# Kernel optimization log

Measured on AMD Instinct MI355X. Metric: run time of the kernel, lower is better.

## Reference

```python
import jax, jax.numpy as jnp
import numpy as np

B, N, D, S, H = 128, 4096, 64, 7, 128  # batch, tokens, slot_size, num_slots, mlp_hidden
EPS = 1e-8
LN_EPS = 1e-5


def _ln(x, w, b):
    m = jnp.mean(x, axis=-1, keepdims=True)
    v = jnp.mean((x - m) ** 2, axis=-1, keepdims=True)
    return (x - m) * jax.lax.rsqrt(v + LN_EPS) * w + b


def setup_inputs() -> dict:
    key = jax.random.key(0)
    ks = jax.random.split(key, 12)
    glorot = lambda k, shape: jax.random.normal(k, shape, jnp.float32) * (2.0 / sum(shape)) ** 0.5
    return {
        "inputs": jax.random.normal(ks[0], (B, N, D), jnp.float32),
        "slots_noise": jax.random.normal(ks[1], (B, S, D), jnp.float32),
        "ln_in_w": jnp.ones((D,), jnp.float32), "ln_in_b": jnp.zeros((D,), jnp.float32),
        "ln_slots_w": jnp.ones((D,), jnp.float32), "ln_slots_b": jnp.zeros((D,), jnp.float32),
        "ln_mlp_w": jnp.ones((D,), jnp.float32), "ln_mlp_b": jnp.zeros((D,), jnp.float32),
        "slots_mu": jax.random.normal(ks[2], (1, 1, D), jnp.float32),
        "slots_log_sigma": jax.random.normal(ks[3], (1, 1, D), jnp.float32) * 0.1,
        "Wq": glorot(ks[4], (D, D)), "Wk": glorot(ks[5], (D, D)), "Wv": glorot(ks[6], (D, D)),
        "W_ih": glorot(ks[7], (3 * D, D)), "W_hh": glorot(ks[8], (3 * D, D)),
        "b_ih": jnp.zeros((3 * D,), jnp.float32), "b_hh": jnp.zeros((3 * D,), jnp.float32),
        "mlp_W1": glorot(ks[9], (H, D)), "mlp_b1": jnp.zeros((H,), jnp.float32),
        "mlp_W2": glorot(ks[10], (D, H)), "mlp_b2": jnp.zeros((D,), jnp.float32),
        "num_iterations": 3,
    }


def reference(inputs, slots_noise, ln_in_w, ln_in_b, ln_slots_w, ln_slots_b,
              ln_mlp_w, ln_mlp_b, slots_mu, slots_log_sigma, Wq, Wk, Wv,
              W_ih, W_hh, b_ih, b_hh, mlp_W1, mlp_b1, mlp_W2, mlp_b2,
              num_iterations):
    d = inputs.shape[-1]
    x = _ln(inputs, ln_in_w, ln_in_b)            # [B,N,D]
    k = x @ Wk.T                                  # [B,N,D]
    v = x @ Wv.T                                  # [B,N,D]
    slots = slots_mu + jnp.exp(slots_log_sigma) * slots_noise  # [B,S,D]
    scale = d ** -0.5
    for _ in range(num_iterations):
        slots_prev = slots
        s = _ln(slots, ln_slots_w, ln_slots_b)
        q = (s @ Wq.T) * scale                    # [B,S,D]
        logits = jnp.einsum('bnd,bsd->bns', k, q) # [B,N,S]
        attn = jax.nn.softmax(logits, axis=-1) + EPS   # softmax over slots
        attn = attn / jnp.sum(attn, axis=-2, keepdims=True)  # renorm over tokens
        updates = jnp.einsum('bns,bnd->bsd', attn, v)  # [B,S,D]
        # GRUCell (torch semantics)
        gi = updates @ W_ih.T + b_ih              # [B,S,3D]
        gh = slots_prev @ W_hh.T + b_hh
        i_r, i_z, i_n = jnp.split(gi, 3, axis=-1)
        h_r, h_z, h_n = jnp.split(gh, 3, axis=-1)
        r = jax.nn.sigmoid(i_r + h_r)
        z = jax.nn.sigmoid(i_z + h_z)
        n = jnp.tanh(i_n + r * h_n)
        slots = (1.0 - z) * n + z * slots_prev
        m = _ln(slots, ln_mlp_w, ln_mlp_b)
        slots = slots + (jax.nn.relu(m @ mlp_W1.T + mlp_b1) @ mlp_W2.T + mlp_b2)
    return slots
```

## Files before the change

kernel.cpp:

```cpp
#include <hip/hip_runtime.h>


#define Nn 4096
#define NCH 16

typedef _Float16 f16;
typedef _Float16 f16x8 __attribute__((ext_vector_type(8)));
typedef _Float16 f16x4 __attribute__((ext_vector_type(4)));
typedef float    f32x4 __attribute__((ext_vector_type(4)));

#define MFMA16(a,b,c) __builtin_amdgcn_mfma_f32_16x16x16f16(a,b,c,0,0,0)
#define MFMA32(a,b,c) __builtin_amdgcn_mfma_f32_16x16x32_f16(a,b,c,0,0,0)
#define LGKM0() asm volatile("s_waitcnt lgkmcnt(0)" ::: "memory")

#if __has_builtin(__builtin_amdgcn_rcpf)
#define RCPF(x) __builtin_amdgcn_rcpf(x)
#else
#define RCPF(x) (1.0f/(x))
#endif

static __device__ __forceinline__ float dot4(f32x4 a, f32x4 b) {
  return a.x*b.x + a.y*b.y + a.z*b.z + a.w*b.w;
}

__global__ __launch_bounds__(256) void k_init(
    const float* __restrict__ noise, const float* __restrict__ mu,
    const float* __restrict__ ls, const float* __restrict__ Wq,
    const float* __restrict__ Wk, float* __restrict__ slots,
    float* __restrict__ Mt)
{
  int bk = blockIdx.x, t = threadIdx.x;
  if (bk < 56) {
    int i = bk*1024 + t*4;
    int d = i & 63;
    f32x4 nz = *(const f32x4*)(noise + i);
    f32x4 m4 = *(const f32x4*)(mu + d);
    f32x4 l4 = *(const f32x4*)(ls + d);
    f32x4 o;
    o.x = m4.x + expf(l4.x)*nz.x; o.y = m4.y + expf(l4.y)*nz.y;
    o.z = m4.z + expf(l4.z)*nz.z; o.w = m4.w + expf(l4.w)*nz.w;
    *(f32x4*)(slots + i) = o;
  } else {
    int idx = (bk-56)*256 + t;
    int d = idx >> 6, e = idx & 63;
    float a = 0.f;
    for (int dd = 0; dd < 64; dd++)
      a += Wk[dd*64 + d] * Wq[dd*64 + e];
    Mt[idx] = a * 0.125f;
  }
}

static __device__ __forceinline__ void stageN(
    float (*dst)[68], const float* __restrict__ src, int stride, int sr, int sc)
{
  #pragma unroll
  for (int k = 0; k < 4; k++)
    *(f32x4*)&dst[sr][sc + k*4] = *(const f32x4*)(src + (size_t)sr*stride + sc + k*4);
}

static __device__ __forceinline__ float dot_row(
    const float (*Wl)[68], int d, const float* v)
{
  float a0 = 0.f, a1 = 0.f;
  #pragma unroll
  for (int jc = 0; jc < 16; jc += 2) {
    a0 += dot4(*(const f32x4*)&Wl[d][jc*4],     *(const f32x4*)(v + jc*4));
    a1 += dot4(*(const f32x4*)&Wl[d][jc*4 + 4], *(const f32x4*)(v + jc*4 + 4));
  }
  return a0 + a1;
}

__global__ __launch_bounds__(256) void k_gru(
    const float* __restrict__ part, const float* __restrict__ csp,
    const float* __restrict__ lnw_in, const float* __restrict__ lnb_in,
    const float* __restrict__ Wv,
    const float* __restrict__ W_ih, const float* __restrict__ W_hh,
    const float* __restrict__ b_ih, const float* __restrict__ b_hh,
    const float* __restrict__ lnm_w, const float* __restrict__ lnm_b,
    const float* __restrict__ W1, const float* __restrict__ b1,
    const float* __restrict__ W2, const float* __restrict__ b2,
    const float* __restrict__ lns_w, const float* __restrict__ lns_b,
    const float* __restrict__ Mt,
    float* __restrict__ slots, f16* __restrict__ qkpad,
    float* __restrict__ qkaux, int do_gru, int do_q)
{
  __shared__ __align__(16) float WA[7][64][68];
  __shared__ __align__(16) float updv[4][64];
  __shared__ __align__(16) float u2v [4][64];
  __shared__ __align__(16) float prevv[4][64];
  __shared__ __align__(16) float mlnv[4][64];
  __shared__ __align__(16) float sn2 [4][64];
  __shared__ __align__(16) float hbuf[4][128];
  const int t = threadIdx.x, w = t >> 6, d = t & 63;
  const int wid = blockIdx.x*4 + w;
  const int b = wid / 7, s = wid - b*7;
  const int sr = t >> 2, sc = (t & 3) * 16;

  float out;
  if (do_gru) {
    {
      const float* srcs[7] = { Wv, W_ih, W_ih + 4096, W_ih + 8192,
                               W_hh, W_hh + 4096, W_hh + 8192 };
      #pragma unroll
      for (int i = 0; i < 7; i++) stageN(WA[i], srcs[i], 64, sr, sc);
    }
    float Y = 0.f, alpha = 0.f;
    #pragma unroll
    for (int cx = 0; cx < NCH; cx++) {
      Y     += part[(((size_t)b*NCH + cx)*8 + s)*64 + d];
      alpha += csp [ ((size_t)b*NCH + cx)*8 + s];
    }
    float upd_pre = lnw_in[d]*(Y/alpha) + lnb_in[d];
    float prev = slots[(size_t)wid*64 + d];
    updv[w][d] = upd_pre; prevv[w][d] = prev;
    __syncthreads();

    u2v[w][d] = dot_row(WA[0], d, updv[w]);
    LGKM0();
    float air = b_ih[d]     + dot_row(WA[1], d, u2v[w]);
    float aiz = b_ih[64+d]  + dot_row(WA[2], d, u2v[w]);
    float ain = b_ih[128+d] + dot_row(WA[3], d, u2v[w]);
    float ahr = b_hh[d]     + dot_row(WA[4], d, prevv[w]);
    float ahz = b_hh[64+d]  + dot_row(WA[5], d, prevv[w]);
    float ahn = b_hh[128+d] + dot_row(WA[6], d, prevv[w]);
    __syncthreads();

    stageN(WA[0], W1,        64,  sr, sc);
    stageN(WA[1], W1 + 4096, 64,  sr, sc);
    stageN(WA[2], W2,        128, sr, sc);
    stageN(WA[3], W2 + 64,   128, sr, sc);
    stageN(WA[4], Mt,        64,  sr, sc);

    float r = 1.f/(1.f + __expf(-(air+ahr)));
    float z = 1.f/(1.f + __expf(-(aiz+ahz)));
    float n = tanhf(ain + r*ahn);
    float hnew = (1.f - z)*n + z*prev;

    float s1 = hnew, s2 = hnew*hnew;
    #pragma unroll
    for (int m = 1; m < 64; m <<= 1) {
      s1 += __shfl_xor(s1, m, 64);
      s2 += __shfl_xor(s2, m, 64);
    }
    float mean = s1*(1.f/64.f), var = s2*(1.f/64.f) - mean*mean;
    float mln = (hnew - mean) * rsqrtf(var + 1e-5f) * lnm_w[d] + lnm_b[d];
    mlnv[w][d] = mln;
    __syncthreads();

    float h0 = fmaxf(b1[d]    + dot_row(WA[0], d, mlnv[w]), 0.f);
    float h1 = fmaxf(b1[64+d] + dot_row(WA[1], d, mlnv[w]), 0.f);
    hbuf[w][d] = h0; hbuf[w][64+d] = h1;
    LGKM0();
    out = hnew + b2[d] + dot_row(WA[2], d, hbuf[w])
                       + dot_row(WA[3], d, hbuf[w] + 64);
    slots[(size_t)wid*64 + d] = out;
  } else {
    stageN(WA[4], Mt, 64, sr, sc);
    out = slots[(size_t)wid*64 + d];
    __syncthreads();
  }

  if (do_q) {
    float s1 = out, s2 = out*out;
    #pragma unroll
    for (int m = 1; m < 64; m <<= 1) {
      s1 += __shfl_xor(s1, m, 64);
      s2 += __shfl_xor(s2, m, 64);
    }
    float mean = s1*(1.f/64.f), var = s2*(1.f/64.f) - mean*mean;
    float sv = (out - mean) * rsqrtf(var + 1e-5f) * lns_w[d] + lns_b[d];
    sn2[w][d] = sv;
    LGKM0();

    float qk = dot_row(WA[4], d, sn2[w]);

    float qw = qk * lnw_in[d];
    float bb = qk * lnb_in[d];
    #pragma unroll
    for (int m = 1; m < 64; m <<= 1)
      bb += __shfl_xor(bb, m, 64);
    qkpad[((size_t)b*16 + s)*64 + d] = (f16)qw;
    if (d == 0) qkaux[(size_t)b*16 + s] = bb;
  }
}

static __device__ __forceinline__ void tile_common(
    f16x8 xf0, f16x8 xf1, const f16x8* qkB, float beta,
    f16x8 selLo, f16x8 selHi, bool valid, f32x4* acc, float& csump)
{
  const f32x4 zero4 = {0.f,0.f,0.f,0.f};
  f32x4 lg = zero4;
  lg = MFMA32(xf0, qkB[0], lg);
  lg = MFMA32(xf1, qkB[1], lg);
  float e[4], sm[4];
  #pragma unroll
  for (int j = 0; j < 4; j++) {
    float L = lg[j] + beta;
    e[j] = valid ? __expf(L) : 0.f;
    sm[j] = e[j];
  }
  #pragma unroll
  for (int m = 1; m < 16; m <<= 1)
    #pragma unroll
    for (int j = 0; j < 4; j++) sm[j] += __shfl_xor(sm[j], m, 64);
  f16x4 pp;
  #pragma unroll
  for (int j = 0; j < 4; j++) {
    float p = valid ? (e[j]*RCPF(sm[j]) + 1e-8f) : 0.f;
    csump += p;
    pp[j] = (f16)p;
  }
  #pragma unroll
  for (int nb = 0; nb < 4; nb++) {
    f32x4 tr = MFMA32(nb < 2 ? xf0 : xf1, (nb & 1) ? selHi : selLo, zero4);
    f16x4 xt; xt.x=(f16)tr.x; xt.y=(f16)tr.y; xt.z=(f16)tr.z; xt.w=(f16)tr.w;
    acc[nb] = MFMA16(pp, xt, acc[nb]);
  }
}

__global__ __launch_bounds__(256, 4) void k_attn(
    const float* __restrict__ x_in, const f16* __restrict__ qkpad,
    const float* __restrict__ qkaux, f16* __restrict__ xh,
    float* __restrict__ part, float* __restrict__ csp, int first)
{
  __shared__ __align__(16) float accb[4][8][64];
  __shared__ float ldsc[4][8];
  const int b = blockIdx.y, cx = blockIdx.x;
  const int tid = threadIdx.x;
  const int w = tid >> 6, lane = tid & 63, q = lane >> 4, c = lane & 15;

  f16x8 qkB[2];
  qkB[0] = *(const f16x8*)(qkpad + ((size_t)b*16 + c)*64 + q*8);
  qkB[1] = *(const f16x8*)(qkpad + ((size_t)b*16 + c)*64 + 32 + q*8);
  const float beta = qkaux[(size_t)b*16 + c];

  f16x8 selLo, selHi;
  #pragma unroll
  for (int j = 0; j < 8; j++) {
    selLo[j] = (f16)((( c>>3)    == q && (c&7) == j) ? 1.0f : 0.0f);
    selHi[j] = (f16)(((c>>3) + 2 == q && (c&7) == j) ? 1.0f : 0.0f);
  }

  const f32x4 zero4 = {0.f,0.f,0.f,0.f};
  f32x4 acc[4] = {zero4, zero4, zero4, zero4};
  float csump = 0.f;
  const size_t tok0 = (size_t)b*Nn + (size_t)cx*256 + (size_t)w*64;
  const bool valid = (c < 7);

  if (first) {
    f32x4 nx[4];
    {
      const float* base = x_in + (tok0 + c)*64;
      nx[0] = *(const f32x4*)(base + q*8);
      nx[1] = *(const f32x4*)(base + q*8 + 4);
      nx[2] = *(const f32x4*)(base + 32 + q*8);
      nx[3] = *(const f32x4*)(base + 32 + q*8 + 4);
    }
    #pragma unroll
    for (int t = 0; t < 4; t++) {
      f32x4 xv[4];
      #pragma unroll
      for (int i = 0; i < 4; i++) xv[i] = nx[i];
      if (t < 3) {
        const float* base = x_in + (tok0 + (t+1)*16 + c)*64;
        nx[0] = *(const f32x4*)(base + q*8);
        nx[1] = *(const f32x4*)(base + q*8 + 4);
        nx[2] = *(const f32x4*)(base + 32 + q*8);
        nx[3] = *(const f32x4*)(base + 32 + q*8 + 4);
      }
      float sx  = (xv[0].x+xv[0].y+xv[0].z+xv[0].w) + (xv[1].x+xv[1].y+xv[1].z+xv[1].w)
                + (xv[2].x+xv[2].y+xv[2].z+xv[2].w) + (xv[3].x+xv[3].y+xv[3].z+xv[3].w);
      float sxx = dot4(xv[0],xv[0]) + dot4(xv[1],xv[1])
                + dot4(xv[2],xv[2]) + dot4(xv[3],xv[3]);
      sx  += __shfl_xor(sx, 16, 64);  sx  += __shfl_xor(sx, 32, 64);
      sxx += __shfl_xor(sxx, 16, 64); sxx += __shfl_xor(sxx, 32, 64);
      float mean = sx*(1.f/64.f);
      float rstd = rsqrtf(sxx*(1.f/64.f) - mean*mean + 1e-5f);
      float mr2 = mean * rstd;
      f16x8 xf0, xf1;
      #pragma unroll
      for (int j = 0; j < 4; j++) {
        xf0[j]   = (f16)(xv[0][j]*rstd - mr2);
        xf0[4+j] = (f16)(xv[1][j]*rstd - mr2);
        xf1[j]   = (f16)(xv[2][j]*rstd - mr2);
        xf1[4+j] = (f16)(xv[3][j]*rstd - mr2);
      }
      f16* xo = xh + (tok0 + t*16 + c)*64;
      *(f16x8*)(xo + q*8)      = xf0;
      *(f16x8*)(xo + 32 + q*8) = xf1;

      tile_common(xf0, xf1, qkB, beta, selLo, selHi, valid, acc, csump);
    }
  } else {
    f16x8 L0[4], L1[4];
    #pragma unroll
    for (int t = 0; t < 4; t++) {
      const f16* base = xh + (tok0 + t*16 + c)*64;
      L0[t] = *(const f16x8*)(base + q*8);
      L1[t] = *(const f16x8*)(base + 32 + q*8);
    }
    #pragma unroll
    for (int t = 0; t < 4; t++)
      tile_common(L0[t], L1[t], qkB, beta, selLo, selHi, valid, acc, csump);
  }

  csump += __shfl_xor(csump, 16, 64); csump += __shfl_xor(csump, 32, 64);
  if (q == 0 && c < 7) ldsc[w][c] = csump;
  if (q < 2) {
    #pragma unroll
    for (int nb = 0; nb < 4; nb++)
      #pragma unroll
      for (int r = 0; r < 4; r++)
        accb[w][q*4 + r][nb*16 + c] = acc[nb][r];
  }
  __syncthreads();
  for (int rr = tid; rr < 448; rr += 256) {
    int row = rr >> 6, dd = rr & 63;
    float v = accb[0][row][dd] + accb[1][row][dd]
            + accb[2][row][dd] + accb[3][row][dd];
    part[(((size_t)b*NCH + cx)*8 + row)*64 + dd] = v;
  }
  if (tid < 7) {
    csp[((size_t)b*NCH + cx)*8 + tid] =
        ldsc[0][tid] + ldsc[1][tid] + ldsc[2][tid] + ldsc[3][tid];
  }
}

extern "C" void kernel_launch(void* const* d_in, const int* in_sizes, int n_in,
                              void* d_out, int out_size, void* d_ws, size_t ws_size,
                              hipStream_t stream) {
  const float* inputs  = (const float*)d_in[0];
  const float* noise   = (const float*)d_in[1];
  const float* ln_in_w = (const float*)d_in[2];
  const float* ln_in_b = (const float*)d_in[3];
  const float* ln_sl_w = (const float*)d_in[4];
  const float* ln_sl_b = (const float*)d_in[5];
  const float* ln_ml_w = (const float*)d_in[6];
  const float* ln_ml_b = (const float*)d_in[7];
  const float* mu   = (const float*)d_in[8];
  const float* ls   = (const float*)d_in[9];
  const float* Wq   = (const float*)d_in[10];
  const float* Wk   = (const float*)d_in[11];
  const float* Wv   = (const float*)d_in[12];
  const float* W_ih = (const float*)d_in[13];
  const float* W_hh = (const float*)d_in[14];
  const float* b_ih = (const float*)d_in[15];
  const float* b_hh = (const float*)d_in[16];
  const float* W1 = (const float*)d_in[17];
  const float* b1 = (const float*)d_in[18];
  const float* W2 = (const float*)d_in[19];
  const float* b2 = (const float*)d_in[20];

  float* slots = (float*)d_out;

  const size_t PART_OFF = 0;
  const size_t CSP_OFF  = PART_OFF + 4194304;
  const size_t QK_OFF   = CSP_OFF  + 65536;
  const size_t QA_OFF   = QK_OFF   + 262144;
  const size_t MT_OFF   = QA_OFF   + 8192;
  const size_t XH_OFF   = MT_OFF   + 16384;
  const size_t NEED     = XH_OFF   + 67108864;
  if (ws_size < NEED) return;

  char* ws = (char*)d_ws;
  float* part  = (float*)(ws + PART_OFF);
  float* csp   = (float*)(ws + CSP_OFF);
  f16*   qkpad = (f16*)  (ws + QK_OFF);
  float* qkaux = (float*)(ws + QA_OFF);
  float* Mt    = (float*)(ws + MT_OFF);
  f16*   xh    = (f16*)  (ws + XH_OFF);

  k_init<<<72, 256, 0, stream>>>(noise, mu, ls, Wq, Wk, slots, Mt);
  k_gru<<<224, 256, 0, stream>>>(part, csp, ln_in_w, ln_in_b, Wv,
                                 W_ih, W_hh, b_ih, b_hh, ln_ml_w, ln_ml_b,
                                 W1, b1, W2, b2, ln_sl_w, ln_sl_b, Mt,
                                 slots, qkpad, qkaux, 0, 1);
  dim3 ga(NCH, 128);
  for (int it = 0; it < 3; it++) {
    k_attn<<<ga, 256, 0, stream>>>(inputs, qkpad, qkaux, xh, part, csp,
                                   it == 0 ? 1 : 0);
    k_gru<<<224, 256, 0, stream>>>(part, csp, ln_in_w, ln_in_b, Wv,
                                   W_ih, W_hh, b_ih, b_hh, ln_ml_w, ln_ml_b,
                                   W1, b1, W2, b2, ln_sl_w, ln_sl_b, Mt,
                                   slots, qkpad, qkaux, 1, it < 2 ? 1 : 0);
  }
}
```

Baseline: 318.0 us.

## Fuse init, attention and GRU iterations into one persistent per-batch kernel

Replaces the eight launches (init, GRU/q, then attention and GRU three times) with a single kernel of 128 blocks of 1024 threads, one block per batch element. Each block computes Mt, the initial slots, attention over all 4096 tokens and the GRU/MLP update in shared memory, so launch gaps and the global partial-sum round trips go away. In exchange only 128 blocks run, one per batch, on a GPU with more compute units than that. Each block streams its whole token range through 16 waves, and weights are staged one 64x64 matrix at a time behind barriers, with only 7 of 16 waves doing the GRU work.

```diff
diff --git a/kernel.cpp b/kernel.cpp
--- a/kernel.cpp
+++ b/kernel.cpp
@@ -2,7 +2,6 @@
 
 
 #define Nn 4096
-#define NCH 16
 
 typedef _Float16 f16;
 typedef _Float16 f16x8 __attribute__((ext_vector_type(8)));
@@ -23,41 +22,6 @@
   return a.x*b.x + a.y*b.y + a.z*b.z + a.w*b.w;
 }
 
-__global__ __launch_bounds__(256) void k_init(
-    const float* __restrict__ noise, const float* __restrict__ mu,
-    const float* __restrict__ ls, const float* __restrict__ Wq,
-    const float* __restrict__ Wk, float* __restrict__ slots,
-    float* __restrict__ Mt)
-{
-  int bk = blockIdx.x, t = threadIdx.x;
-  if (bk < 56) {
-    int i = bk*1024 + t*4;
-    int d = i & 63;
-    f32x4 nz = *(const f32x4*)(noise + i);
-    f32x4 m4 = *(const f32x4*)(mu + d);
-    f32x4 l4 = *(const f32x4*)(ls + d);
-    f32x4 o;
-    o.x = m4.x + expf(l4.x)*nz.x; o.y = m4.y + expf(l4.y)*nz.y;
-    o.z = m4.z + expf(l4.z)*nz.z; o.w = m4.w + expf(l4.w)*nz.w;
-    *(f32x4*)(slots + i) = o;
-  } else {
-    int idx = (bk-56)*256 + t;
-    int d = idx >> 6, e = idx & 63;
-    float a = 0.f;
-    for (int dd = 0; dd < 64; dd++)
-      a += Wk[dd*64 + d] * Wq[dd*64 + e];
-    Mt[idx] = a * 0.125f;
-  }
-}
-
-static __device__ __forceinline__ void stageN(
-    float (*dst)[68], const float* __restrict__ src, int stride, int sr, int sc)
-{
-  #pragma unroll
-  for (int k = 0; k < 4; k++)
-    *(f32x4*)&dst[sr][sc + k*4] = *(const f32x4*)(src + (size_t)sr*stride + sc + k*4);
-}
-
 static __device__ __forceinline__ float dot_row(
     const float (*Wl)[68], int d, const float* v)
 {
@@ -70,118 +34,25 @@
   return a0 + a1;
 }
 
-__global__ __launch_bounds__(256) void k_gru(
-    const float* __restrict__ part, const float* __restrict__ csp,
-    const float* __restrict__ lnw_in, const float* __restrict__ lnb_in,
-    const float* __restrict__ Wv,
-    const float* __restrict__ W_ih, const float* __restrict__ W_hh,
-    const float* __restrict__ b_ih, const float* __restrict__ b_hh,
-    const float* __restrict__ lnm_w, const float* __restrict__ lnm_b,
-    const float* __restrict__ W1, const float* __restrict__ b1,
-    const float* __restrict__ W2, const float* __restrict__ b2,
-    const float* __restrict__ lns_w, const float* __restrict__ lns_b,
-    const float* __restrict__ Mt,
-    float* __restrict__ slots, f16* __restrict__ qkpad,
-    float* __restrict__ qkaux, int do_gru, int do_q)
-{
-  __shared__ __align__(16) float WA[7][64][68];
-  __shared__ __align__(16) float updv[4][64];
-  __shared__ __align__(16) float u2v [4][64];
-  __shared__ __align__(16) float prevv[4][64];
-  __shared__ __align__(16) float mlnv[4][64];
-  __shared__ __align__(16) float sn2 [4][64];
-  __shared__ __align__(16) float hbuf[4][128];
-  const int t = threadIdx.x, w = t >> 6, d = t & 63;
-  const int wid = blockIdx.x*4 + w;
-  const int b = wid / 7, s = wid - b*7;
-  const int sr = t >> 2, sc = (t & 3) * 16;
-
-  float out;
-  if (do_gru) {
-    {
-      const float* srcs[7] = { Wv, W_ih, W_ih + 4096, W_ih + 8192,
-                               W_hh, W_hh + 4096, W_hh + 8192 };
-      #pragma unroll
-      for (int i = 0; i < 7; i++) stageN(WA[i], srcs[i], 64, sr, sc);
-    }
-    float Y = 0.f, alpha = 0.f;
-    #pragma unroll
-    for (int cx = 0; cx < NCH; cx++) {
-      Y     += part[(((size_t)b*NCH + cx)*8 + s)*64 + d];
-      alpha += csp [ ((size_t)b*NCH + cx)*8 + s];
-    }
-    float upd_pre = lnw_in[d]*(Y/alpha) + lnb_in[d];
-    float prev = slots[(size_t)wid*64 + d];
-    updv[w][d] = upd_pre; prevv[w][d] = prev;
-    __syncthreads();
-
-    u2v[w][d] = dot_row(WA[0], d, updv[w]);
-    LGKM0();
-    float air = b_ih[d]     + dot_row(WA[1], d, u2v[w]);
-    float aiz = b_ih[64+d]  + dot_row(WA[2], d, u2v[w]);
-    float ain = b_ih[128+d] + dot_row(WA[3], d, u2v[w]);
-    float ahr = b_hh[d]     + dot_row(WA[4], d, prevv[w]);
-    float ahz = b_hh[64+d]  + dot_row(WA[5], d, prevv[w]);
-    float ahn = b_hh[128+d] + dot_row(WA[6], d, prevv[w]);
-    __syncthreads();
-
-    stageN(WA[0], W1,        64,  sr, sc);
-    stageN(WA[1], W1 + 4096, 64,  sr, sc);
-    stageN(WA[2], W2,        128, sr, sc);
-    stageN(WA[3], W2 + 64,   128, sr, sc);
-    stageN(WA[4], Mt,        64,  sr, sc);
-
-    float r = 1.f/(1.f + __expf(-(air+ahr)));
-    float z = 1.f/(1.f + __expf(-(aiz+ahz)));
-    float n = tanhf(ain + r*ahn);
-    float hnew = (1.f - z)*n + z*prev;
-
-    float s1 = hnew, s2 = hnew*hnew;
-    #pragma unroll
-    for (int m = 1; m < 64; m <<= 1) {
-      s1 += __shfl_xor(s1, m, 64);
-      s2 += __shfl_xor(s2, m, 64);
-    }
-    float mean = s1*(1.f/64.f), var = s2*(1.f/64.f) - mean*mean;
-    float mln = (hnew - mean) * rsqrtf(var + 1e-5f) * lnm_w[d] + lnm_b[d];
-    mlnv[w][d] = mln;
-    __syncthreads();
-
-    float h0 = fmaxf(b1[d]    + dot_row(WA[0], d, mlnv[w]), 0.f);
-    float h1 = fmaxf(b1[64+d] + dot_row(WA[1], d, mlnv[w]), 0.f);
-    hbuf[w][d] = h0; hbuf[w][64+d] = h1;
-    LGKM0();
-    out = hnew + b2[d] + dot_row(WA[2], d, hbuf[w])
-                       + dot_row(WA[3], d, hbuf[w] + 64);
-    slots[(size_t)wid*64 + d] = out;
-  } else {
-    stageN(WA[4], Mt, 64, sr, sc);
-    out = slots[(size_t)wid*64 + d];
-    __syncthreads();
-  }
-
-  if (do_q) {
-    float s1 = out, s2 = out*out;
-    #pragma unroll
-    for (int m = 1; m < 64; m <<= 1) {
-      s1 += __shfl_xor(s1, m, 64);
-      s2 += __shfl_xor(s2, m, 64);
-    }
-    float mean = s1*(1.f/64.f), var = s2*(1.f/64.f) - mean*mean;
-    float sv = (out - mean) * rsqrtf(var + 1e-5f) * lns_w[d] + lns_b[d];
-    sn2[w][d] = sv;
-    LGKM0();
-
-    float qk = dot_row(WA[4], d, sn2[w]);
-
-    float qw = qk * lnw_in[d];
-    float bb = qk * lnb_in[d];
-    #pragma unroll
-    for (int m = 1; m < 64; m <<= 1)
-      bb += __shfl_xor(bb, m, 64);
-    qkpad[((size_t)b*16 + s)*64 + d] = (f16)qw;
-    if (d == 0) qkaux[(size_t)b*16 + s] = bb;
-  }
+static __device__ __forceinline__ void stage1024(
+    float (*Wl)[68], const float* __restrict__ src, int stride, int sr, int sc4)
+{
+  __syncthreads();
+  *(f32x4*)&Wl[sr][sc4] = *(const f32x4*)(src + (size_t)sr*stride + sc4);
+  __syncthreads();
+}
+
+static __device__ __forceinline__ float ln64(
+    float v, const float* __restrict__ w, const float* __restrict__ bias, int lane)
+{
+  float s1 = v, s2 = v*v;
+  #pragma unroll
+  for (int m = 1; m < 64; m <<= 1) {
+    s1 += __shfl_xor(s1, m, 64);
+    s2 += __shfl_xor(s2, m, 64);
+  }
+  float mean = s1*(1.f/64.f), var = s2*(1.f/64.f) - mean*mean;
+  return (v - mean) * rsqrtf(var + 1e-5f) * w[lane] + bias[lane];
 }
 
 static __device__ __forceinline__ void tile_common(
@@ -218,21 +89,77 @@
   }
 }
 
-__global__ __launch_bounds__(256, 4) void k_attn(
-    const float* __restrict__ x_in, const f16* __restrict__ qkpad,
-    const float* __restrict__ qkaux, f16* __restrict__ xh,
-    float* __restrict__ part, float* __restrict__ csp, int first)
-{
-  __shared__ __align__(16) float accb[4][8][64];
-  __shared__ float ldsc[4][8];
-  const int b = blockIdx.y, cx = blockIdx.x;
-  const int tid = threadIdx.x;
-  const int w = tid >> 6, lane = tid & 63, q = lane >> 4, c = lane & 15;
-
-  f16x8 qkB[2];
-  qkB[0] = *(const f16x8*)(qkpad + ((size_t)b*16 + c)*64 + q*8);
-  qkB[1] = *(const f16x8*)(qkpad + ((size_t)b*16 + c)*64 + 32 + q*8);
-  const float beta = qkaux[(size_t)b*16 + c];
+__global__ __launch_bounds__(1024) void k_all(
+    const float* __restrict__ x_in, const float* __restrict__ noise,
+    const float* __restrict__ lnw_in, const float* __restrict__ lnb_in,
+    const float* __restrict__ lns_w, const float* __restrict__ lns_b,
+    const float* __restrict__ lnm_w, const float* __restrict__ lnm_b,
+    const float* __restrict__ mu, const float* __restrict__ ls,
+    const float* __restrict__ Wq, const float* __restrict__ Wk,
+    const float* __restrict__ Wv,
+    const float* __restrict__ W_ih, const float* __restrict__ W_hh,
+    const float* __restrict__ b_ih, const float* __restrict__ b_hh,
+    const float* __restrict__ W1, const float* __restrict__ b1,
+    const float* __restrict__ W2, const float* __restrict__ b2,
+    float* __restrict__ slots_out, f16* __restrict__ xh)
+{
+  __shared__ __align__(16) float Wl[64][68];
+  __shared__ __align__(16) float Mt_l[64][68];
+  __shared__ __align__(16) float accb[16][8][64];
+  __shared__ float ldsc[16][8];
+  __shared__ float alphas[8];
+  __shared__ __align__(16) f16 qkw_l[16][72];
+  __shared__ float beta_l[16];
+  __shared__ __align__(16) float updv[7][64];
+  __shared__ __align__(16) float u2v [7][64];
+  __shared__ __align__(16) float prevv[7][64];
+  __shared__ __align__(16) float mlnv[7][64];
+  __shared__ __align__(16) float sn2 [7][64];
+  __shared__ __align__(16) float hbuf[7][128];
+
+  const int b = blockIdx.x, tid = threadIdx.x;
+  const int wv = tid >> 6, lane = tid & 63;
+  const int q = lane >> 4, c = lane & 15;
+  const int sr = tid >> 4, sc4 = (tid & 15) * 4;
+
+  *(f32x4*)&Wl[sr][sc4]   = *(const f32x4*)(Wk + sr*64 + sc4);
+  *(f32x4*)&Mt_l[sr][sc4] = *(const f32x4*)(Wq + sr*64 + sc4);
+  for (int i = tid; i < 16*72; i += 1024) ((f16*)qkw_l)[i] = (f16)0.f;
+  if (tid >= 7 && tid < 16) beta_l[tid] = 0.f;
+  __syncthreads();
+  float mtv[4];
+  {
+    #pragma unroll
+    for (int j = 0; j < 4; j++) mtv[j] = 0.f;
+    for (int dd = 0; dd < 64; dd++) {
+      float wk = Wl[dd][sr];
+      const float* wq = &Mt_l[dd][sc4];
+      #pragma unroll
+      for (int j = 0; j < 4; j++) mtv[j] += wk * wq[j];
+    }
+  }
+  __syncthreads();
+  #pragma unroll
+  for (int j = 0; j < 4; j++) Mt_l[sr][sc4 + j] = mtv[j] * 0.125f;
+
+  float prev = 0.f;
+  if (wv < 7)
+    prev = mu[lane] + __expf(ls[lane]) * noise[(size_t)(b*7 + wv)*64 + lane];
+  __syncthreads();
+
+  if (wv < 7) {
+    float sv = ln64(prev, lns_w, lns_b, lane);
+    sn2[wv][lane] = sv;
+    LGKM0();
+    float qk = dot_row(Mt_l, lane, sn2[wv]);
+    float qw = qk * lnw_in[lane];
+    float bb = qk * lnb_in[lane];
+    #pragma unroll
+    for (int m = 1; m < 64; m <<= 1) bb += __shfl_xor(bb, m, 64);
+    qkw_l[wv][lane] = (f16)qw;
+    if (lane == 0) beta_l[wv] = bb;
+  }
+  __syncthreads();
 
   f16x8 selLo, selHi;
   #pragma unroll
@@ -240,89 +167,163 @@
     selLo[j] = (f16)((( c>>3)    == q && (c&7) == j) ? 1.0f : 0.0f);
     selHi[j] = (f16)(((c>>3) + 2 == q && (c&7) == j) ? 1.0f : 0.0f);
   }
-
+  const bool valid = (c < 7);
   const f32x4 zero4 = {0.f,0.f,0.f,0.f};
-  f32x4 acc[4] = {zero4, zero4, zero4, zero4};
-  float csump = 0.f;
-  const size_t tok0 = (size_t)b*Nn + (size_t)cx*256 + (size_t)w*64;
-  const bool valid = (c < 7);
-
-  if (first) {
-    f32x4 nx[4];
-    {
-      const float* base = x_in + (tok0 + c)*64;
-      nx[0] = *(const f32x4*)(base + q*8);
-      nx[1] = *(const f32x4*)(base + q*8 + 4);
-      nx[2] = *(const f32x4*)(base + 32 + q*8);
-      nx[3] = *(const f32x4*)(base + 32 + q*8 + 4);
-    }
-    #pragma unroll
-    for (int t = 0; t < 4; t++) {
-      f32x4 xv[4];
-      #pragma unroll
-      for (int i = 0; i < 4; i++) xv[i] = nx[i];
-      if (t < 3) {
-        const float* base = x_in + (tok0 + (t+1)*16 + c)*64;
+
+  for (int it = 0; it < 3; ++it) {
+    f16x8 qkB[2];
+    qkB[0] = *(const f16x8*)&qkw_l[c][q*8];
+    qkB[1] = *(const f16x8*)&qkw_l[c][32 + q*8];
+    const float beta = beta_l[c];
+
+    f32x4 acc[4] = {zero4, zero4, zero4, zero4};
+    float csump = 0.f;
+    const size_t tok0 = (size_t)b*Nn + (size_t)wv*256;
+
+    if (it == 0) {
+      f32x4 nx[4];
+      {
+        const float* base = x_in + (tok0 + c)*64;
         nx[0] = *(const f32x4*)(base + q*8);
         nx[1] = *(const f32x4*)(base + q*8 + 4);
         nx[2] = *(const f32x4*)(base + 32 + q*8);
         nx[3] = *(const f32x4*)(base + 32 + q*8 + 4);
       }
-      float sx  = (xv[0].x+xv[0].y+xv[0].z+xv[0].w) + (xv[1].x+xv[1].y+xv[1].z+xv[1].w)
-                + (xv[2].x+xv[2].y+xv[2].z+xv[2].w) + (xv[3].x+xv[3].y+xv[3].z+xv[3].w);
-      float sxx = dot4(xv[0],xv[0]) + dot4(xv[1],xv[1])
-                + dot4(xv[2],xv[2]) + dot4(xv[3],xv[3]);
-      sx  += __shfl_xor(sx, 16, 64);  sx  += __shfl_xor(sx, 32, 64);
-      sxx += __shfl_xor(sxx, 16, 64); sxx += __shfl_xor(sxx, 32, 64);
-      float mean = sx*(1.f/64.f);
-      float rstd = rsqrtf(sxx*(1.f/64.f) - mean*mean + 1e-5f);
-      float mr2 = mean * rstd;
-      f16x8 xf0, xf1;
+      for (int t = 0; t < 16; t++) {
+        f32x4 xv[4];
+        #pragma unroll
+        for (int i = 0; i < 4; i++) xv[i] = nx[i];
+        if (t < 15) {
+          const float* base = x_in + (tok0 + (t+1)*16 + c)*64;
+          nx[0] = *(const f32x4*)(base + q*8);
+          nx[1] = *(const f32x4*)(base + q*8 + 4);
+          nx[2] = *(const f32x4*)(base + 32 + q*8);
+          nx[3] = *(const f32x4*)(base + 32 + q*8 + 4);
+        }
+        float sx  = (xv[0].x+xv[0].y+xv[0].z+xv[0].w) + (xv[1].x+xv[1].y+xv[1].z+xv[1].w)
+                  + (xv[2].x+xv[2].y+xv[2].z+xv[2].w) + (xv[3].x+xv[3].y+xv[3].z+xv[3].w);
+        float sxx = dot4(xv[0],xv[0]) + dot4(xv[1],xv[1])
+                  + dot4(xv[2],xv[2]) + dot4(xv[3],xv[3]);
+        sx  += __shfl_xor(sx, 16, 64);  sx  += __shfl_xor(sx, 32, 64);
+        sxx += __shfl_xor(sxx, 16, 64); sxx += __shfl_xor(sxx, 32, 64);
+        float mean = sx*(1.f/64.f);
+        float rstd = rsqrtf(sxx*(1.f/64.f) - mean*mean + 1e-5f);
+        float mr2 = mean * rstd;
+        f16x8 xf0, xf1;
+        #pragma unroll
+        for (int j = 0; j < 4; j++) {
+          xf0[j]   = (f16)(xv[0][j]*rstd - mr2);
+          xf0[4+j] = (f16)(xv[1][j]*rstd - mr2);
+          xf1[j]   = (f16)(xv[2][j]*rstd - mr2);
+          xf1[4+j] = (f16)(xv[3][j]*rstd - mr2);
+        }
+        f16* xo = xh + (tok0 + t*16 + c)*64;
+        *(f16x8*)(xo + q*8)      = xf0;
+        *(f16x8*)(xo + 32 + q*8) = xf1;
+        tile_common(xf0, xf1, qkB, beta, selLo, selHi, valid, acc, csump);
+      }
+    } else {
+      for (int g = 0; g < 4; g++) {
+        f16x8 L0[4], L1[4];
+        #pragma unroll
+        for (int tt = 0; tt < 4; tt++) {
+          const f16* base = xh + (tok0 + (g*4 + tt)*16 + c)*64;
+          L0[tt] = *(const f16x8*)(base + q*8);
+          L1[tt] = *(const f16x8*)(base + 32 + q*8);
+        }
+        #pragma unroll
+        for (int tt = 0; tt < 4; tt++)
+          tile_common(L0[tt], L1[tt], qkB, beta, selLo, selHi, valid, acc, csump);
+      }
+    }
+
+    csump += __shfl_xor(csump, 16, 64); csump += __shfl_xor(csump, 32, 64);
+    if (q == 0 && c < 7) ldsc[wv][c] = csump;
+    if (q < 2) {
       #pragma unroll
-      for (int j = 0; j < 4; j++) {
-        xf0[j]   = (f16)(xv[0][j]*rstd - mr2);
-        xf0[4+j] = (f16)(xv[1][j]*rstd - mr2);
-        xf1[j]   = (f16)(xv[2][j]*rstd - mr2);
-        xf1[4+j] = (f16)(xv[3][j]*rstd - mr2);
+      for (int nb = 0; nb < 4; nb++)
+        #pragma unroll
+        for (int rr = 0; rr < 4; rr++)
+          accb[wv][q*4 + rr][nb*16 + c] = acc[nb][rr];
+    }
+    if (wv < 7) prevv[wv][lane] = prev;
+    __syncthreads();
+
+    if (tid < 7) {
+      float a = 0.f;
+      #pragma unroll
+      for (int w2 = 0; w2 < 16; w2++) a += ldsc[w2][tid];
+      alphas[tid] = a;
+    }
+    __syncthreads();
+    if (tid < 448) {
+      int row = tid >> 6, d = tid & 63;
+      float Y = 0.f;
+      #pragma unroll
+      for (int w2 = 0; w2 < 16; w2++) Y += accb[w2][row][d];
+      updv[row][d] = lnw_in[d]*(Y / alphas[row]) + lnb_in[d];
+    }
+
+    stage1024(Wl, Wv, 64, sr, sc4);
+    if (wv < 7) { u2v[wv][lane] = dot_row(Wl, lane, updv[wv]); }
+
+    stage1024(Wl, W_ih,        64, sr, sc4);
+    float air = 0.f, aiz = 0.f, ain = 0.f, ahr = 0.f, ahz = 0.f, ahn = 0.f;
+    if (wv < 7) air = b_ih[lane]     + dot_row(Wl, lane, u2v[wv]);
+    stage1024(Wl, W_ih + 4096, 64, sr, sc4);
+    if (wv < 7) aiz = b_ih[64+lane]  + dot_row(Wl, lane, u2v[wv]);
+    stage1024(Wl, W_ih + 8192, 64, sr, sc4);
+    if (wv < 7) ain = b_ih[128+lane] + dot_row(Wl, lane, u2v[wv]);
+    stage1024(Wl, W_hh,        64, sr, sc4);
+    if (wv < 7) ahr = b_hh[lane]     + dot_row(Wl, lane, prevv[wv]);
+    stage1024(Wl, W_hh + 4096, 64, sr, sc4);
+    if (wv < 7) ahz = b_hh[64+lane]  + dot_row(Wl, lane, prevv[wv]);
+    stage1024(Wl, W_hh + 8192, 64, sr, sc4);
+    if (wv < 7) ahn = b_hh[128+lane] + dot_row(Wl, lane, prevv[wv]);
+
+    float hnew = 0.f;
+    if (wv < 7) {
+      float rg = 1.f/(1.f + __expf(-(air+ahr)));
+      float zg = 1.f/(1.f + __expf(-(aiz+ahz)));
+      float ng = tanhf(ain + rg*ahn);
+      hnew = (1.f - zg)*ng + zg*prev;
+      mlnv[wv][lane] = ln64(hnew, lnm_w, lnm_b, lane);
+    }
+
+    stage1024(Wl, W1,        64, sr, sc4);
+    float h0 = 0.f, h1 = 0.f;
+    if (wv < 7) h0 = fmaxf(b1[lane]    + dot_row(Wl, lane, mlnv[wv]), 0.f);
+    stage1024(Wl, W1 + 4096, 64, sr, sc4);
+    if (wv < 7) {
+      h1 = fmaxf(b1[64+lane] + dot_row(Wl, lane, mlnv[wv]), 0.f);
+      hbuf[wv][lane] = h0; hbuf[wv][64+lane] = h1;
+    }
+    stage1024(Wl, W2,      128, sr, sc4);
+    float out = 0.f;
+    if (wv < 7) out = hnew + b2[lane] + dot_row(Wl, lane, hbuf[wv]);
+    stage1024(Wl, W2 + 64, 128, sr, sc4);
+    if (wv < 7) {
+      out += dot_row(Wl, lane, hbuf[wv] + 64);
+      prev = out;
+    }
+
+    if (it == 2) {
+      if (wv < 7) slots_out[(size_t)(b*7 + wv)*64 + lane] = out;
+    } else {
+      if (wv < 7) {
+        float sv = ln64(out, lns_w, lns_b, lane);
+        sn2[wv][lane] = sv;
+        LGKM0();
+        float qk = dot_row(Mt_l, lane, sn2[wv]);
+        float qw = qk * lnw_in[lane];
+        float bb = qk * lnb_in[lane];
+        #pragma unroll
+        for (int m = 1; m < 64; m <<= 1) bb += __shfl_xor(bb, m, 64);
+        qkw_l[wv][lane] = (f16)qw;
+        if (lane == 0) beta_l[wv] = bb;
       }
-      f16* xo = xh + (tok0 + t*16 + c)*64;
-      *(f16x8*)(xo + q*8)      = xf0;
-      *(f16x8*)(xo + 32 + q*8) = xf1;
-
-      tile_common(xf0, xf1, qkB, beta, selLo, selHi, valid, acc, csump);
-    }
-  } else {
-    f16x8 L0[4], L1[4];
-    #pragma unroll
-    for (int t = 0; t < 4; t++) {
-      const f16* base = xh + (tok0 + t*16 + c)*64;
-      L0[t] = *(const f16x8*)(base + q*8);
-      L1[t] = *(const f16x8*)(base + 32 + q*8);
-    }
-    #pragma unroll
-    for (int t = 0; t < 4; t++)
-      tile_common(L0[t], L1[t], qkB, beta, selLo, selHi, valid, acc, csump);
-  }
-
-  csump += __shfl_xor(csump, 16, 64); csump += __shfl_xor(csump, 32, 64);
-  if (q == 0 && c < 7) ldsc[w][c] = csump;
-  if (q < 2) {
-    #pragma unroll
-    for (int nb = 0; nb < 4; nb++)
-      #pragma unroll
-      for (int r = 0; r < 4; r++)
-        accb[w][q*4 + r][nb*16 + c] = acc[nb][r];
-  }
-  __syncthreads();
-  for (int rr = tid; rr < 448; rr += 256) {
-    int row = rr >> 6, dd = rr & 63;
-    float v = accb[0][row][dd] + accb[1][row][dd]
-            + accb[2][row][dd] + accb[3][row][dd];
-    part[(((size_t)b*NCH + cx)*8 + row)*64 + dd] = v;
-  }
-  if (tid < 7) {
-    csp[((size_t)b*NCH + cx)*8 + tid] =
-        ldsc[0][tid] + ldsc[1][tid] + ldsc[2][tid] + ldsc[3][tid];
+      __syncthreads();
+    }
   }
 }
 
@@ -353,35 +354,12 @@
 
   float* slots = (float*)d_out;
 
-  const size_t PART_OFF = 0;
-  const size_t CSP_OFF  = PART_OFF + 4194304;
-  const size_t QK_OFF   = CSP_OFF  + 65536;
-  const size_t QA_OFF   = QK_OFF   + 262144;
-  const size_t MT_OFF   = QA_OFF   + 8192;
-  const size_t XH_OFF   = MT_OFF   + 16384;
-  const size_t NEED     = XH_OFF   + 67108864;
+  const size_t NEED = 67108864;
   if (ws_size < NEED) return;
-
-  char* ws = (char*)d_ws;
-  float* part  = (float*)(ws + PART_OFF);
-  float* csp   = (float*)(ws + CSP_OFF);
-  f16*   qkpad = (f16*)  (ws + QK_OFF);
-  float* qkaux = (float*)(ws + QA_OFF);
-  float* Mt    = (float*)(ws + MT_OFF);
-  f16*   xh    = (f16*)  (ws + XH_OFF);
-
-  k_init<<<72, 256, 0, stream>>>(noise, mu, ls, Wq, Wk, slots, Mt);
-  k_gru<<<224, 256, 0, stream>>>(part, csp, ln_in_w, ln_in_b, Wv,
-                                 W_ih, W_hh, b_ih, b_hh, ln_ml_w, ln_ml_b,
-                                 W1, b1, W2, b2, ln_sl_w, ln_sl_b, Mt,
-                                 slots, qkpad, qkaux, 0, 1);
-  dim3 ga(NCH, 128);
-  for (int it = 0; it < 3; it++) {
-    k_attn<<<ga, 256, 0, stream>>>(inputs, qkpad, qkaux, xh, part, csp,
-                                   it == 0 ? 1 : 0);
-    k_gru<<<224, 256, 0, stream>>>(part, csp, ln_in_w, ln_in_b, Wv,
-                                   W_ih, W_hh, b_ih, b_hh, ln_ml_w, ln_ml_b,
-                                   W1, b1, W2, b2, ln_sl_w, ln_sl_b, Mt,
-                                   slots, qkpad, qkaux, 1, it < 2 ? 1 : 0);
-  }
-}
+  f16* xh = (f16*)d_ws;
+
+  k_all<<<128, 1024, 0, stream>>>(
+      inputs, noise, ln_in_w, ln_in_b, ln_sl_w, ln_sl_b, ln_ml_w, ln_ml_b,
+      mu, ls, Wq, Wk, Wv, W_ih, W_hh, b_ih, b_hh, W1, b1, W2, b2,
+      slots, xh);
+}
```

Result: slower. 431.0 us (+35.5%).
